# Performance work log

Hardware: AMD Instinct MI355X
Metric: run time of the kernel (lower is better)

The kernel has to match this reference:

```python
import jax, jax.numpy as jnp
import numpy as np


def setup_inputs() -> dict:
    key = jax.random.key(0)
    ks = jax.random.split(key, 9)
    B, C, H, W = 4, 256, 128, 128
    d = C // 8
    x = jax.random.normal(ks[0], (B, C, H, W), jnp.float32)
    wq = jax.random.normal(ks[1], (d, C), jnp.float32) * 0.05
    bq = jax.random.normal(ks[2], (d,), jnp.float32) * 0.05
    wk = jax.random.normal(ks[3], (d, C), jnp.float32) * 0.05
    bk = jax.random.normal(ks[4], (d,), jnp.float32) * 0.05
    wv = jax.random.normal(ks[5], (d, C), jnp.float32) * 0.05
    bv = jax.random.normal(ks[6], (d,), jnp.float32) * 0.05
    wp = jax.random.normal(ks[7], (C, d, 3, 3), jnp.float32) * 0.05
    gamma = jax.random.normal(ks[8], (1,), jnp.float32)
    return dict(x=x, wq=wq, bq=bq, wk=wk, bk=bk, wv=wv, bv=bv, wp=wp, gamma=gamma)


def reference(x, wq, bq, wk, bk, wv, bv, wp, gamma):
    B, C, H, W = x.shape
    d = wq.shape[0]  # C // 8
    N = H * W
    # 1x1 convs expressed as channel matmuls
    q = jnp.einsum('bchw,dc->bdhw', x, wq) + bq[None, :, None, None]
    k = jnp.einsum('bchw,dc->bdhw', x, wk) + bk[None, :, None, None]
    v = jnp.einsum('bchw,dc->bdhw', x, wv) + bv[None, :, None, None]
    Q = q.reshape(B, d, N)
    K = k.reshape(B, d, N)
    V = v.reshape(B, d, N)
    # channel-channel energy: [B, d, d]
    energy = jnp.einsum('bdn,ben->bde', Q, K)
    energy_new = jnp.max(energy, axis=-1, keepdims=True) - energy
    attention = jax.nn.softmax(energy_new, axis=-1)
    out = jnp.einsum('bde,ben->bdn', attention, V).reshape(B, d, H, W)
    # 3x3 conv (no bias) + exact GELU
    out = jax.lax.conv_general_dilated(
        out, wp, window_strides=(1, 1), padding='SAME',
        dimension_numbers=('NCHW', 'OIHW', 'NCHW'))
    out = jax.nn.gelu(out, approximate=False)
    return gamma[0] * out + x
```

## Files before the change

### kernel.cpp

```cpp
#include <hip/hip_runtime.h>
#include <hip/hip_bf16.h>
#include <math.h>

#define BB 4
#define CC 256
#define HH 128
#define WW 128
#define NN (HH*WW)
#define DD 32

#define AOT_CI   44
#define AOT_ROWE (130*AOT_CI)
#define AOT_IMGE (130*AOT_ROWE)
#define AOT_BYTES ((size_t)BB*AOT_IMGE*2)
#define AOT_ALLOC (AOT_BYTES + 1024)

#define WT_BYTES (9*256*AOT_CI*2)

#define PATCH_SZ 45760
#define WSLAB    22528
#define CONV_LDS (PATCH_SZ + 2*WSLAB)
#define EPI_PITCH 260

#define ASWZ_BYTES 98304
#define QKVP 260
#define QKV_LDS 131584

typedef __attribute__((ext_vector_type(8)))  short bf16x8;
typedef __attribute__((ext_vector_type(4)))  float f32x4;
typedef __attribute__((ext_vector_type(16))) float f32x16;

__device__ inline void async_copy16(void* lds, const void* g) {
    __builtin_amdgcn_global_load_lds(
        (const __attribute__((address_space(1))) unsigned int*)g,
        (__attribute__((address_space(3))) unsigned int*)lds, 16, 0, 0);
}

__device__ inline unsigned short f2bf(float f) {
    __hip_bfloat16 h = __float2bfloat16(f);
    return *reinterpret_cast<unsigned short*>(&h);
}

__device__ inline void split2(float v, unsigned short& h, unsigned short& l) {
    __hip_bfloat16 hb = __float2bfloat16(v);
    float r = v - __bfloat162float(hb);
    __hip_bfloat16 lb = __float2bfloat16(r);
    h = *reinterpret_cast<unsigned short*>(&hb);
    l = *reinterpret_cast<unsigned short*>(&lb);
}

__device__ inline unsigned int packsplit(float v) {
    unsigned int fb = __float_as_uint(v);
    unsigned int hb = fb & 0xFFFF0000u;
    float r = v - __uint_as_float(hb);
    unsigned int lb = __float_as_uint(r) >> 16;
    return (hb >> 16) | (lb << 16);
}

__device__ inline bf16x8 ld_frag8(const char* p) {
    union { bf16x8 v; short4 h[2]; } u;
    u.h[0] = *(const short4*)(p);
    u.h[1] = *(const short4*)(p + 8);
    return u.v;
}

__device__ inline float gelu_fast(float v) {
    float a = fabsf(v) * 0.70710678118654752f;
    float t = __fdividef(1.0f, fmaf(0.3275911f, a, 1.0f));
    float p = t * fmaf(t, fmaf(t, fmaf(t, fmaf(t, 1.061405429f, -1.453152027f),
                                       1.421413741f), -0.284496736f), 0.254829592f);
    float e = 1.0f - p * __expf(-a * a);
    float erfv = (v < 0.0f) ? -e : e;
    return 0.5f * v * (1.0f + erfv);
}

__global__ __launch_bounds__(256) void prep_kernel(
    const float* __restrict__ wp, unsigned short* __restrict__ Wt,
    const float* __restrict__ wq, const float* __restrict__ wk,
    const float* __restrict__ wv, unsigned short* __restrict__ Aswz,
    unsigned short* __restrict__ AOT)
{
    const int blk = blockIdx.x;
    if (blk < 288) {
        int i = blk*256 + threadIdx.x;
        int kk = i / (256*32);
        int r  = i % (256*32);
        int co = r >> 5, ci = r & 31;
        float v = wp[((size_t)co*32 + ci)*9 + kk];
        Wt[((size_t)kk*256 + co)*AOT_CI + ci] = f2bf(v);
    } else if (blk < 480) {
        int i = (blk-288)*256 + threadIdx.x;
        int j    = i & 7;
        int lane = (i >> 3) & 63;
        int q9   = i >> 9;
        int cf   = q9 % 3;
        int t    = q9 / 3;
        int hl   = t & 1;
        int s    = t >> 1;
        int row  = cf*32 + (lane & 31);
        int c    = s*16 + (lane >> 5)*8 + j;
        float w  = (row < 32) ? wq[row*256 + c]
                 : (row < 64) ? wk[(row-32)*256 + c]
                              : wv[(row-64)*256 + c];
        unsigned short h, l;
        split2(w, h, l);
        Aswz[i] = hl ? l : h;
    } else {
        int idx = (blk-480)*256 + threadIdx.x;
        if (idx < BB*22704) {
            int b = idx / 22704;
            int r = idx % 22704;
            size_t off;
            if (r < 11440) {
                int row = (r < 5720) ? 0 : 129;
                int e   = (r < 5720) ? r : r - 5720;
                off = (size_t)b*AOT_IMGE + (size_t)row*AOT_ROWE + e;
            } else {
                int r2 = r - 11440;
                int rr = r2 / 88 + 1;
                int w2 = r2 % 88;
                int col = (w2 < 44) ? 0 : 129;
                int ci  = (w2 < 44) ? w2 : w2 - 44;
                off = (size_t)b*AOT_IMGE + (size_t)rr*AOT_ROWE
                    + (size_t)col*AOT_CI + ci;
            }
            AOT[off] = 0;
        }
    }
}

__global__ __launch_bounds__(512, 1) void qkv_mfma_kernel(
    const float* __restrict__ x, const unsigned short* __restrict__ Aswz,
    const float* __restrict__ bq, const float* __restrict__ bk,
    const float* __restrict__ bv,
    float* __restrict__ Vout, float* __restrict__ Ep)
{
    __shared__ __align__(16) char lds[QKV_LDS];
    const int b    = blockIdx.y;
    const int s    = blockIdx.x;
    const int n0   = s * 256;
    const int tid  = threadIdx.x;
    const int w    = tid >> 6;
    const int lane = tid & 63;
    const int l31  = lane & 31;
    const int lh   = lane >> 5;
    const int ch_a = tid >> 6;
    const int f4   = tid & 63;

    for (int i = tid; i < 6144; i += 512)
        async_copy16(lds + i*16, (const char*)Aswz + i*16);
    float* biasL = (float*)(lds + 131072);
    if (tid < 96)
        biasL[tid] = (tid < 32) ? bq[tid] : (tid < 64) ? bk[tid-32] : bv[tid-64];

    unsigned int* stg[2] = { (unsigned int*)(lds + 98304),
                             (unsigned int*)(lds + 114688) };
    const float* xb = x + (size_t)b*CC*NN + n0 + f4*4;

    f32x16 acc0 = {0}, acc1 = {0}, acc2 = {0};

    float4 va0, vb0, va1, vb1, va2, vb2;
    #define LOADX(VA, VB, R) do { \
        VA = *(const float4*)(xb + (size_t)((R)*16 + ch_a    )*NN); \
        VB = *(const float4*)(xb + (size_t)((R)*16 + ch_a + 8)*NN); } while (0)
    #define PACKW(BUF, VA, VB) do { \
        uint4 ua, ub; \
        ua.x = packsplit((VA).x); ua.y = packsplit((VA).y); \
        ua.z = packsplit((VA).z); ua.w = packsplit((VA).w); \
        ub.x = packsplit((VB).x); ub.y = packsplit((VB).y); \
        ub.z = packsplit((VB).z); ub.w = packsplit((VB).w); \
        *(uint4*)((BUF) + (ch_a    )*256 + f4*4) = ua; \
        *(uint4*)((BUF) + (ch_a + 8)*256 + f4*4) = ub; } while (0)

    LOADX(va0, vb0, 0);
    LOADX(va1, vb1, 1);
    LOADX(va2, vb2, 2);
    PACKW(stg[0], va0, vb0);
    __syncthreads();

    #pragma unroll
    for (int r = 0; r < 16; ++r) {
        {
            const unsigned int* bufc = stg[r & 1];
            unsigned int u[8];
            #pragma unroll
            for (int j = 0; j < 8; ++j)
                u[j] = bufc[(lh*8 + j)*256 + 32*w + l31];
            union { bf16x8 v; unsigned int d[4]; } B1, B2;
            #pragma unroll
            for (int dq = 0; dq < 4; ++dq) {
                B1.d[dq] = (u[2*dq] & 0xFFFFu)      | (u[2*dq+1] << 16);
                B2.d[dq] = (u[2*dq] >> 16)          | (u[2*dq+1] & 0xFFFF0000u);
            }
            #pragma unroll
            for (int cf = 0; cf < 3; ++cf) {
                bf16x8 ah = *(const bf16x8*)(lds + (((r*6 +     cf)*64) + lane)*16);
                bf16x8 al = *(const bf16x8*)(lds + (((r*6 + 3 + cf)*64) + lane)*16);
                f32x16* ac = (cf == 0) ? &acc0 : (cf == 1) ? &acc1 : &acc2;
                *ac = __builtin_amdgcn_mfma_f32_32x32x16_bf16(ah, B1.v, *ac, 0, 0, 0);
                *ac = __builtin_amdgcn_mfma_f32_32x32x16_bf16(ah, B2.v, *ac, 0, 0, 0);
                *ac = __builtin_amdgcn_mfma_f32_32x32x16_bf16(al, B1.v, *ac, 0, 0, 0);
                *ac = __builtin_amdgcn_mfma_f32_32x32x16_bf16(al, B2.v, *ac, 0, 0, 0);
            }
        }
        if (r < 15) {
            if ((r+1) % 3 == 0)      PACKW(stg[(r+1) & 1], va0, vb0);
            else if ((r+1) % 3 == 1) PACKW(stg[(r+1) & 1], va1, vb1);
            else                     PACKW(stg[(r+1) & 1], va2, vb2);
        }
        if (r + 3 < 16) {
            if ((r+3) % 3 == 0)      LOADX(va0, vb0, r+3);
            else if ((r+3) % 3 == 1) LOADX(va1, vb1, r+3);
            else                     LOADX(va2, vb2, r+3);
        }
        __syncthreads();
    }

    float* qk = (float*)lds;
    #pragma unroll
    for (int r = 0; r < 16; ++r) {
        const int rsub = (r & 3) + 8*(r >> 2) + 4*lh;
        const int col  = 32*w + l31;
        qk[rsub*QKVP + col]      = acc0[r] + biasL[rsub];
        qk[(32+rsub)*QKVP + col] = acc1[r] + biasL[32 + rsub];
        Vout[((size_t)b*DD + rsub)*NN + n0 + col] = acc2[r] + biasL[64 + rsub];
    }
    __syncthreads();

    const int d  = tid >> 4;
    const int e2 = tid & 15;
    const float* qrow = qk + d*QKVP;
    float s0 = 0.f, s1 = 0.f;
    for (int n4 = 0; n4 < 256; n4 += 4) {
        float4 qv = *(const float4*)(qrow + n4);
        float4 ka = *(const float4*)(qk + (32 + e2)*QKVP + n4);
        float4 kb = *(const float4*)(qk + (48 + e2)*QKVP + n4);
        s0 += qv.x*ka.x + qv.y*ka.y + qv.z*ka.z + qv.w*ka.w;
        s1 += qv.x*kb.x + qv.y*kb.y + qv.z*kb.z + qv.w*kb.w;
    }
    float* ep = Ep + ((size_t)s*BB + b)*1024;
    ep[d*32 + e2]      = s0;
    ep[d*32 + e2 + 16] = s1;
    #undef LOADX
    #undef PACKW
}

__global__ __launch_bounds__(1024) void softmax_kernel(
    const float* __restrict__ Ep, float* __restrict__ attT)
{
    const int b = blockIdx.x;
    const int e = threadIdx.x, d = threadIdx.y;
    float s = 0.f;
    #pragma unroll 8
    for (int p = 0; p < 64; ++p)
        s += Ep[((size_t)p * BB + b) * (DD * DD) + d * DD + e];
    float nv = -s;
    float m = nv;
    for (int off = 16; off > 0; off >>= 1) m = fmaxf(m, __shfl_xor(m, off, 32));
    float pe = expf(nv - m);
    float su = pe;
    for (int off = 16; off > 0; off >>= 1) su += __shfl_xor(su, off, 32);
    attT[(size_t)b * (DD * DD) + e * DD + d] = pe / su;
}

__global__ __launch_bounds__(256) void pv_kernel(
    const float* __restrict__ V, const float* __restrict__ attT,
    unsigned short* __restrict__ AOT)
{
    __shared__ float Vs[DD][128];
    __shared__ float at4[DD][DD];
    const int b  = blockIdx.y;
    const int n0 = blockIdx.x * 128;
    const int tid = threadIdx.x;
    for (int i = tid; i < 1024; i += 256) {
        int r = i >> 5, c4 = i & 31;
        *(float4*)&Vs[r][c4*4] =
            *(const float4*)(V + ((size_t)b*DD + r)*NN + n0 + c4*4);
    }
    for (int i = tid; i < 1024; i += 256)
        at4[i >> 5][i & 31] = attT[(size_t)b*1024 + i];
    __syncthreads();
    const int nl = tid & 127;
    const int dg = tid >> 7;
    float acc[16];
    #pragma unroll
    for (int k = 0; k < 16; ++k) acc[k] = 0.f;
    #pragma unroll 4
    for (int e = 0; e < DD; ++e) {
        float v = Vs[e][nl];
        const float4* ar = (const float4*)&at4[e][dg*16];
        #pragma unroll
        for (int q = 0; q < 4; ++q) {
            float4 a = ar[q];
            acc[4*q+0] += a.x * v; acc[4*q+1] += a.y * v;
            acc[4*q+2] += a.z * v; acc[4*q+3] += a.w * v;
        }
    }
    const int n = n0 + nl;
    const int h = n >> 7, ww = n & 127;
    unsigned short* dst = AOT + (size_t)b*AOT_IMGE + (size_t)(h+1)*AOT_ROWE
                              + (size_t)(ww+1)*AOT_CI + dg*16;
    #pragma unroll
    for (int q = 0; q < 4; ++q) {
        ushort4 u;
        u.x = f2bf(acc[4*q+0]); u.y = f2bf(acc[4*q+1]);
        u.z = f2bf(acc[4*q+2]); u.w = f2bf(acc[4*q+3]);
        *(ushort4*)(dst + 4*q) = u;
    }
}

__global__ __launch_bounds__(512, 1) void conv_kernel(
    const unsigned short* __restrict__ AOT, const unsigned short* __restrict__ Wt,
    const float* __restrict__ gammap, const float* __restrict__ x,
    float* __restrict__ out)
{
    __shared__ __align__(16) char lds[CONV_LDS];
    const int b   = blockIdx.y;
    const int h0  = blockIdx.x * 2;
    const int tid = threadIdx.x;
    const int wid = tid >> 6;
    const int lane = tid & 63;
    const int l15 = lane & 15;
    const int lj  = lane >> 4;
    const int wn  = wid & 1;
    const int wc  = wid >> 1;

    const char* psrc = (const char*)(AOT + (size_t)b*AOT_IMGE + (size_t)h0*AOT_ROWE);
    for (int i = tid; i < PATCH_SZ/16; i += 512)
        async_copy16(lds + i*16, psrc + i*16);
    for (int i = tid; i < WSLAB/16; i += 512)
        async_copy16(lds + PATCH_SZ + i*16, (const char*)Wt + i*16);
    __syncthreads();

    f32x4 acc[4][8];
    #pragma unroll
    for (int cf = 0; cf < 4; ++cf)
        #pragma unroll
        for (int nf = 0; nf < 8; ++nf)
            acc[cf][nf] = (f32x4){0.f, 0.f, 0.f, 0.f};

    for (int kk = 0; kk < 9; ++kk) {
        if (kk < 8) {
            const char* wsrc = (const char*)Wt + (size_t)(kk+1)*WSLAB;
            char* wdst = lds + PATCH_SZ + ((kk+1)&1)*WSLAB;
            for (int i = tid; i < WSLAB/16; i += 512)
                async_copy16(wdst + i*16, wsrc + i*16);
        }
        const int kh = kk / 3, kw = kk % 3;
        const char* wbase = lds + PATCH_SZ + (kk&1)*WSLAB;
        bf16x8 af[4];
        #pragma unroll
        for (int cf = 0; cf < 4; ++cf)
            af[cf] = ld_frag8(wbase + (wc*64 + cf*16 + l15)*88 + lj*16);
        #pragma unroll
        for (int nf = 0; nf < 8; ++nf) {
            const int cell = (wn + kh)*130 + nf*16 + l15 + kw;
            const bf16x8 bfr = ld_frag8(lds + cell*88 + lj*16);
            #pragma unroll
            for (int cf = 0; cf < 4; ++cf)
                acc[cf][nf] = __builtin_amdgcn_mfma_f32_16x16x32_bf16(
                    af[cf], bfr, acc[cf][nf], 0, 0, 0);
        }
        __syncthreads();
    }

    const float g0 = gammap[0];
    float* lf = (float*)lds;
    for (int k = 0; k < 4; ++k) {
        if (wc == k) {
            #pragma unroll
            for (int cf = 0; cf < 4; ++cf) {
                const int rl = cf*16 + 4*lj;
                #pragma unroll
                for (int nf = 0; nf < 8; ++nf) {
                    const int col = wn*128 + nf*16 + l15;
                    #pragma unroll
                    for (int j = 0; j < 4; ++j)
                        lf[(rl + j)*EPI_PITCH + col] = acc[cf][nf][j];
                }
            }
        }
        __syncthreads();
        #pragma unroll
        for (int it = 0; it < 8; ++it) {
            const int idx = tid + it*512;
            const int row = idx >> 6, c4 = idx & 63;
            const int co  = k*64 + row;
            const size_t g = ((size_t)b*CC + co)*NN + (size_t)h0*WW + c4*4;
            float4 v  = *(const float4*)(lf + row*EPI_PITCH + c4*4);
            float4 xv = *(const float4*)(x + g);
            float4 o;
            o.x = g0*gelu_fast(v.x) + xv.x;
            o.y = g0*gelu_fast(v.y) + xv.y;
            o.z = g0*gelu_fast(v.z) + xv.z;
            o.w = g0*gelu_fast(v.w) + xv.w;
            *(float4*)(out + g) = o;
        }
        __syncthreads();
    }
}

extern "C" void kernel_launch(void* const* d_in, const int* in_sizes, int n_in,
                              void* d_out, int out_size, void* d_ws, size_t ws_size,
                              hipStream_t stream)
{
    const float* x  = (const float*)d_in[0];
    const float* wq = (const float*)d_in[1];
    const float* bq = (const float*)d_in[2];
    const float* wk = (const float*)d_in[3];
    const float* bk = (const float*)d_in[4];
    const float* wv = (const float*)d_in[5];
    const float* bv = (const float*)d_in[6];
    const float* wp = (const float*)d_in[7];
    const float* gm = (const float*)d_in[8];
    float* out = (float*)d_out;

    float* Vbuf = out;

    char* ws = (char*)d_ws;
    unsigned short* AOT  = (unsigned short*)ws;
    unsigned short* Wt   = (unsigned short*)(ws + AOT_ALLOC);
    unsigned short* Aswz = (unsigned short*)(ws + AOT_ALLOC + WT_BYTES);
    float* Ep  = (float*)(ws + AOT_ALLOC + WT_BYTES + ASWZ_BYTES);
    float* ATT = Ep + (size_t)64*BB*1024;

    prep_kernel    <<<dim3(1024), 256, 0, stream>>>(wp, Wt, wq, wk, wv, Aswz, AOT);
    qkv_mfma_kernel<<<dim3(64, BB), 512, 0, stream>>>(x, Aswz, bq, bk, bv, Vbuf, Ep);
    softmax_kernel <<<dim3(BB), dim3(32, 32), 0, stream>>>(Ep, ATT);
    pv_kernel      <<<dim3(128, BB), 256, 0, stream>>>(Vbuf, ATT, AOT);
    conv_kernel    <<<dim3(64, BB), 512, 0, stream>>>(AOT, Wt, gm, x, out);
}
```

Baseline: 79.89 us.

## Fuse QKV, softmax and PV into one cooperative kernel with grid sync

Merges the QKV projection, channel softmax and attention-times-V kernels into one cooperative kernel that uses a grid-wide barrier after writing partial energies. V stays in registers instead of making a round trip through global memory, and two kernel launches go away. Each block recomputes the softmax for its batch redundantly from the partial sums, then applies the attention matrix to its register-resident V tile and writes bf16 into the padded conv input. The prep grid size also changes. The change depends on all 256 blocks being co-resident for the grid sync, and launch bounds are raised to 2 blocks per CU even though the kernel uses about 131KB of LDS per block.

Result: slower. 161.8 us (+102.5%).

```diff
diff --git a/kernel.cpp b/kernel.cpp
--- a/kernel.cpp
+++ b/kernel.cpp
@@ -1,5 +1,6 @@
 #include <hip/hip_runtime.h>
 #include <hip/hip_bf16.h>
+#include <hip/hip_cooperative_groups.h>
 #include <math.h>
 
 #define BB 4
@@ -29,6 +30,8 @@
 typedef __attribute__((ext_vector_type(8)))  short bf16x8;
 typedef __attribute__((ext_vector_type(4)))  float f32x4;
 typedef __attribute__((ext_vector_type(16))) float f32x16;
+
+namespace cg = cooperative_groups;
 
 __device__ inline void async_copy16(void* lds, const void* g) {
     __builtin_amdgcn_global_load_lds(
@@ -129,11 +132,11 @@
     }
 }
 
-__global__ __launch_bounds__(512, 1) void qkv_mfma_kernel(
+__global__ __launch_bounds__(512, 2) void fused_attn_kernel(
     const float* __restrict__ x, const unsigned short* __restrict__ Aswz,
     const float* __restrict__ bq, const float* __restrict__ bk,
     const float* __restrict__ bv,
-    float* __restrict__ Vout, float* __restrict__ Ep)
+    float* __restrict__ Ep, unsigned short* __restrict__ AOT)
 {
     __shared__ __align__(16) char lds[QKV_LDS];
     const int b    = blockIdx.y;
@@ -189,8 +192,8 @@
             union { bf16x8 v; unsigned int d[4]; } B1, B2;
             #pragma unroll
             for (int dq = 0; dq < 4; ++dq) {
-                B1.d[dq] = (u[2*dq] & 0xFFFFu)      | (u[2*dq+1] << 16);
-                B2.d[dq] = (u[2*dq] >> 16)          | (u[2*dq+1] & 0xFFFF0000u);
+                B1.d[dq] = (u[2*dq] & 0xFFFFu) | (u[2*dq+1] << 16);
+                B2.d[dq] = (u[2*dq] >> 16)     | (u[2*dq+1] & 0xFFFF0000u);
             }
             #pragma unroll
             for (int cf = 0; cf < 3; ++cf) {
@@ -215,6 +218,8 @@
         }
         __syncthreads();
     }
+    #undef LOADX
+    #undef PACKW
 
     float* qk = (float*)lds;
     #pragma unroll
@@ -223,89 +228,85 @@
         const int col  = 32*w + l31;
         qk[rsub*QKVP + col]      = acc0[r] + biasL[rsub];
         qk[(32+rsub)*QKVP + col] = acc1[r] + biasL[32 + rsub];
-        Vout[((size_t)b*DD + rsub)*NN + n0 + col] = acc2[r] + biasL[64 + rsub];
     }
     __syncthreads();
 
-    const int d  = tid >> 4;
-    const int e2 = tid & 15;
-    const float* qrow = qk + d*QKVP;
-    float s0 = 0.f, s1 = 0.f;
-    for (int n4 = 0; n4 < 256; n4 += 4) {
-        float4 qv = *(const float4*)(qrow + n4);
-        float4 ka = *(const float4*)(qk + (32 + e2)*QKVP + n4);
-        float4 kb = *(const float4*)(qk + (48 + e2)*QKVP + n4);
-        s0 += qv.x*ka.x + qv.y*ka.y + qv.z*ka.z + qv.w*ka.w;
-        s1 += qv.x*kb.x + qv.y*kb.y + qv.z*kb.z + qv.w*kb.w;
-    }
-    float* ep = Ep + ((size_t)s*BB + b)*1024;
-    ep[d*32 + e2]      = s0;
-    ep[d*32 + e2 + 16] = s1;
-    #undef LOADX
-    #undef PACKW
-}
-
-__global__ __launch_bounds__(1024) void softmax_kernel(
-    const float* __restrict__ Ep, float* __restrict__ attT)
-{
-    const int b = blockIdx.x;
-    const int e = threadIdx.x, d = threadIdx.y;
-    float s = 0.f;
-    #pragma unroll 8
-    for (int p = 0; p < 64; ++p)
-        s += Ep[((size_t)p * BB + b) * (DD * DD) + d * DD + e];
-    float nv = -s;
-    float m = nv;
-    for (int off = 16; off > 0; off >>= 1) m = fmaxf(m, __shfl_xor(m, off, 32));
-    float pe = expf(nv - m);
-    float su = pe;
-    for (int off = 16; off > 0; off >>= 1) su += __shfl_xor(su, off, 32);
-    attT[(size_t)b * (DD * DD) + e * DD + d] = pe / su;
-}
-
-__global__ __launch_bounds__(256) void pv_kernel(
-    const float* __restrict__ V, const float* __restrict__ attT,
-    unsigned short* __restrict__ AOT)
-{
-    __shared__ float Vs[DD][128];
-    __shared__ float at4[DD][DD];
-    const int b  = blockIdx.y;
-    const int n0 = blockIdx.x * 128;
-    const int tid = threadIdx.x;
-    for (int i = tid; i < 1024; i += 256) {
-        int r = i >> 5, c4 = i & 31;
-        *(float4*)&Vs[r][c4*4] =
-            *(const float4*)(V + ((size_t)b*DD + r)*NN + n0 + c4*4);
-    }
-    for (int i = tid; i < 1024; i += 256)
-        at4[i >> 5][i & 31] = attT[(size_t)b*1024 + i];
+    {
+        const int d  = tid >> 4;
+        const int e2 = tid & 15;
+        const float* qrow = qk + d*QKVP;
+        float s0 = 0.f, s1 = 0.f;
+        for (int n4 = 0; n4 < 256; n4 += 4) {
+            float4 qv = *(const float4*)(qrow + n4);
+            float4 ka = *(const float4*)(qk + (32 + e2)*QKVP + n4);
+            float4 kb = *(const float4*)(qk + (48 + e2)*QKVP + n4);
+            s0 += qv.x*ka.x + qv.y*ka.y + qv.z*ka.z + qv.w*ka.w;
+            s1 += qv.x*kb.x + qv.y*kb.y + qv.z*kb.z + qv.w*kb.w;
+        }
+        float* ep = Ep + ((size_t)s*BB + b)*1024;
+        ep[d*32 + e2]      = s0;
+        ep[d*32 + e2 + 16] = s1;
+    }
+
+    __threadfence();
+    cg::this_grid().sync();
+
+    float* at4 = (float*)(lds + 98304);
+    {
+        float e0s = 0.f, e1s = 0.f;
+        #pragma unroll 8
+        for (int p = 0; p < 64; ++p) {
+            float2 v = *(const float2*)(Ep + ((size_t)p*BB + b)*1024 + 2*tid);
+            e0s += v.x; e1s += v.y;
+        }
+        float nv0 = -e0s, nv1 = -e1s;
+        float m = fmaxf(nv0, nv1);
+        for (int off = 8; off > 0; off >>= 1) m = fmaxf(m, __shfl_xor(m, off, 16));
+        float p0 = expf(nv0 - m), p1 = expf(nv1 - m);
+        float su = p0 + p1;
+        for (int off = 8; off > 0; off >>= 1) su += __shfl_xor(su, off, 16);
+        const float inv = 1.0f / su;
+        const int d = tid >> 4;
+        const int e = 2*(tid & 15);
+        at4[e*36 + d]     = p0 * inv;
+        at4[(e+1)*36 + d] = p1 * inv;
+    }
     __syncthreads();
-    const int nl = tid & 127;
-    const int dg = tid >> 7;
-    float acc[16];
-    #pragma unroll
-    for (int k = 0; k < 16; ++k) acc[k] = 0.f;
-    #pragma unroll 4
-    for (int e = 0; e < DD; ++e) {
-        float v = Vs[e][nl];
-        const float4* ar = (const float4*)&at4[e][dg*16];
+
+    {
+        float accd[32];
+        #pragma unroll
+        for (int d = 0; d < 32; ++d) accd[d] = 0.f;
+        #pragma unroll
+        for (int r = 0; r < 16; ++r) {
+            const int rsub = (r & 3) + 8*(r >> 2) + 4*lh;
+            const float v = acc2[r] + biasL[64 + rsub];
+            const float4* ar = (const float4*)(at4 + rsub*36);
+            #pragma unroll
+            for (int dq = 0; dq < 8; ++dq) {
+                float4 a = ar[dq];
+                accd[4*dq+0] += a.x * v; accd[4*dq+1] += a.y * v;
+                accd[4*dq+2] += a.z * v; accd[4*dq+3] += a.w * v;
+            }
+        }
+        #pragma unroll
+        for (int d = 0; d < 32; ++d)
+            accd[d] += __shfl_xor(accd[d], 32);
+        float fin[16];
+        #pragma unroll
+        for (int j = 0; j < 16; ++j)
+            fin[j] = lh ? accd[16 + j] : accd[j];
+        const int n  = n0 + 32*w + l31;
+        const int h  = n >> 7, ww = n & 127;
+        unsigned short* dst = AOT + (size_t)b*AOT_IMGE + (size_t)(h+1)*AOT_ROWE
+                                  + (size_t)(ww+1)*AOT_CI + 16*lh;
         #pragma unroll
         for (int q = 0; q < 4; ++q) {
-            float4 a = ar[q];
-            acc[4*q+0] += a.x * v; acc[4*q+1] += a.y * v;
-            acc[4*q+2] += a.z * v; acc[4*q+3] += a.w * v;
-        }
-    }
-    const int n = n0 + nl;
-    const int h = n >> 7, ww = n & 127;
-    unsigned short* dst = AOT + (size_t)b*AOT_IMGE + (size_t)(h+1)*AOT_ROWE
-                              + (size_t)(ww+1)*AOT_CI + dg*16;
-    #pragma unroll
-    for (int q = 0; q < 4; ++q) {
-        ushort4 u;
-        u.x = f2bf(acc[4*q+0]); u.y = f2bf(acc[4*q+1]);
-        u.z = f2bf(acc[4*q+2]); u.w = f2bf(acc[4*q+3]);
-        *(ushort4*)(dst + 4*q) = u;
+            ushort4 u;
+            u.x = f2bf(fin[4*q+0]); u.y = f2bf(fin[4*q+1]);
+            u.z = f2bf(fin[4*q+2]); u.w = f2bf(fin[4*q+3]);
+            *(ushort4*)(dst + 4*q) = u;
+        }
     }
 }
 
@@ -415,18 +416,20 @@
     const float* gm = (const float*)d_in[8];
     float* out = (float*)d_out;
 
-    float* Vbuf = out;
-
     char* ws = (char*)d_ws;
     unsigned short* AOT  = (unsigned short*)ws;
     unsigned short* Wt   = (unsigned short*)(ws + AOT_ALLOC);
     unsigned short* Aswz = (unsigned short*)(ws + AOT_ALLOC + WT_BYTES);
-    float* Ep  = (float*)(ws + AOT_ALLOC + WT_BYTES + ASWZ_BYTES);
-    float* ATT = Ep + (size_t)64*BB*1024;
-
-    prep_kernel    <<<dim3(1024), 256, 0, stream>>>(wp, Wt, wq, wk, wv, Aswz, AOT);
-    qkv_mfma_kernel<<<dim3(64, BB), 512, 0, stream>>>(x, Aswz, bq, bk, bv, Vbuf, Ep);
-    softmax_kernel <<<dim3(BB), dim3(32, 32), 0, stream>>>(Ep, ATT);
-    pv_kernel      <<<dim3(128, BB), 256, 0, stream>>>(Vbuf, ATT, AOT);
-    conv_kernel    <<<dim3(64, BB), 512, 0, stream>>>(AOT, Wt, gm, x, out);
-}
+    float* Ep = (float*)(ws + AOT_ALLOC + WT_BYTES + ASWZ_BYTES);
+
+    prep_kernel<<<dim3(835), 256, 0, stream>>>(wp, Wt, wq, wk, wv, Aswz, AOT);
+
+    {
+        void* args[] = { (void*)&x, (void*)&Aswz, (void*)&bq, (void*)&bk,
+                         (void*)&bv, (void*)&Ep, (void*)&AOT };
+        hipLaunchCooperativeKernel((void*)fused_attn_kernel,
+                                   dim3(64, BB), dim3(512), args, 0, stream);
+    }
+
+    conv_kernel<<<dim3(64, BB), 512, 0, stream>>>(AOT, Wt, gm, x, out);
+}
```

## Use per-wave staging buffers in QKV kernel to drop per-iteration barriers

Applied to the files above, without the earlier changes.

The QKV MFMA kernel now gives each wave a private double-buffered LDS slab holding only the 32 spatial columns it consumes. The per-iteration __syncthreads in the 16-step channel loop can therefore be removed, and the next global load of x is issued before the MFMA work. The intent is to cut block-wide barrier stalls and improve overlap of loads with compute. It relies on in-wave ordering of LDS writes and reads. The prep kernel grid also shrinks from 1024 to 835 blocks, which is only safe if its work partition matches.

New measurement: 79.88 us. Within noise of the previous version (-0.0%).

```diff
diff --git a/kernel.cpp b/kernel.cpp
--- a/kernel.cpp
+++ b/kernel.cpp
@@ -144,8 +144,8 @@
     const int lane = tid & 63;
     const int l31  = lane & 31;
     const int lh   = lane >> 5;
-    const int ch_a = tid >> 6;
-    const int f4   = tid & 63;
+    const int chl  = lane >> 3;
+    const int nq   = lane & 7;
 
     for (int i = tid; i < 6144; i += 512)
         async_copy16(lds + i*16, (const char*)Aswz + i*16);
@@ -153,44 +153,49 @@
     if (tid < 96)
         biasL[tid] = (tid < 32) ? bq[tid] : (tid < 64) ? bk[tid-32] : bv[tid-64];
 
-    unsigned int* stg[2] = { (unsigned int*)(lds + 98304),
-                             (unsigned int*)(lds + 114688) };
-    const float* xb = x + (size_t)b*CC*NN + n0 + f4*4;
+    char* mybuf = lds + 98304 + w*4096;
+    const float* xq4 = x + (size_t)b*CC*NN + n0 + 32*w + nq*4;
 
     f32x16 acc0 = {0}, acc1 = {0}, acc2 = {0};
 
-    float4 va0, vb0, va1, vb1, va2, vb2;
+    float4 sa0, sb0, sa1, sb1, sa2, sb2;
     #define LOADX(VA, VB, R) do { \
-        VA = *(const float4*)(xb + (size_t)((R)*16 + ch_a    )*NN); \
-        VB = *(const float4*)(xb + (size_t)((R)*16 + ch_a + 8)*NN); } while (0)
-    #define PACKW(BUF, VA, VB) do { \
+        VA = *(const float4*)(xq4 + (size_t)((R)*16 + chl    )*NN); \
+        VB = *(const float4*)(xq4 + (size_t)((R)*16 + 8 + chl)*NN); } while (0)
+    #define PACKW(R, VA, VB) do { \
+        unsigned int* bp = (unsigned int*)(mybuf + ((R) & 1)*2048); \
         uint4 ua, ub; \
         ua.x = packsplit((VA).x); ua.y = packsplit((VA).y); \
         ua.z = packsplit((VA).z); ua.w = packsplit((VA).w); \
         ub.x = packsplit((VB).x); ub.y = packsplit((VB).y); \
         ub.z = packsplit((VB).z); ub.w = packsplit((VB).w); \
-        *(uint4*)((BUF) + (ch_a    )*256 + f4*4) = ua; \
-        *(uint4*)((BUF) + (ch_a + 8)*256 + f4*4) = ub; } while (0)
-
-    LOADX(va0, vb0, 0);
-    LOADX(va1, vb1, 1);
-    LOADX(va2, vb2, 2);
-    PACKW(stg[0], va0, vb0);
+        *(uint4*)(bp + (chl    )*32 + nq*4) = ua; \
+        *(uint4*)(bp + (8 + chl)*32 + nq*4) = ub; } while (0)
+
+    LOADX(sa0, sb0, 0);
+    LOADX(sa1, sb1, 1);
+    LOADX(sa2, sb2, 2);
+    PACKW(0, sa0, sb0);
     __syncthreads();
 
     #pragma unroll
     for (int r = 0; r < 16; ++r) {
+        if (r + 3 < 16) {
+            if ((r+3) % 3 == 0)      LOADX(sa0, sb0, r+3);
+            else if ((r+3) % 3 == 1) LOADX(sa1, sb1, r+3);
+            else                     LOADX(sa2, sb2, r+3);
+        }
         {
-            const unsigned int* bufc = stg[r & 1];
+            const unsigned int* bufc = (const unsigned int*)(mybuf + (r & 1)*2048);
             unsigned int u[8];
             #pragma unroll
             for (int j = 0; j < 8; ++j)
-                u[j] = bufc[(lh*8 + j)*256 + 32*w + l31];
+                u[j] = bufc[(lh*8 + j)*32 + l31];
             union { bf16x8 v; unsigned int d[4]; } B1, B2;
             #pragma unroll
             for (int dq = 0; dq < 4; ++dq) {
-                B1.d[dq] = (u[2*dq] & 0xFFFFu)      | (u[2*dq+1] << 16);
-                B2.d[dq] = (u[2*dq] >> 16)          | (u[2*dq+1] & 0xFFFF0000u);
+                B1.d[dq] = (u[2*dq] & 0xFFFFu) | (u[2*dq+1] << 16);
+                B2.d[dq] = (u[2*dq] >> 16)     | (u[2*dq+1] & 0xFFFF0000u);
             }
             #pragma unroll
             for (int cf = 0; cf < 3; ++cf) {
@@ -203,19 +208,16 @@
                 *ac = __builtin_amdgcn_mfma_f32_32x32x16_bf16(al, B2.v, *ac, 0, 0, 0);
             }
         }
-        if (r < 15) {
-            if ((r+1) % 3 == 0)      PACKW(stg[(r+1) & 1], va0, vb0);
-            else if ((r+1) % 3 == 1) PACKW(stg[(r+1) & 1], va1, vb1);
-            else                     PACKW(stg[(r+1) & 1], va2, vb2);
-        }
-        if (r + 3 < 16) {
-            if ((r+3) % 3 == 0)      LOADX(va0, vb0, r+3);
-            else if ((r+3) % 3 == 1) LOADX(va1, vb1, r+3);
-            else                     LOADX(va2, vb2, r+3);
-        }
-        __syncthreads();
-    }
-
+        if (r + 1 < 16) {
+            if ((r+1) % 3 == 0)      PACKW(r+1, sa0, sb0);
+            else if ((r+1) % 3 == 1) PACKW(r+1, sa1, sb1);
+            else                     PACKW(r+1, sa2, sb2);
+        }
+    }
+    #undef LOADX
+    #undef PACKW
+
+    __syncthreads();
     float* qk = (float*)lds;
     #pragma unroll
     for (int r = 0; r < 16; ++r) {
@@ -241,8 +243,6 @@
     float* ep = Ep + ((size_t)s*BB + b)*1024;
     ep[d*32 + e2]      = s0;
     ep[d*32 + e2 + 16] = s1;
-    #undef LOADX
-    #undef PACKW
 }
 
 __global__ __launch_bounds__(1024) void softmax_kernel(
@@ -424,7 +424,7 @@
     float* Ep  = (float*)(ws + AOT_ALLOC + WT_BYTES + ASWZ_BYTES);
     float* ATT = Ep + (size_t)64*BB*1024;
 
-    prep_kernel    <<<dim3(1024), 256, 0, stream>>>(wp, Wt, wq, wk, wv, Aswz, AOT);
+    prep_kernel    <<<dim3(835), 256, 0, stream>>>(wp, Wt, wq, wk, wv, Aswz, AOT);
     qkv_mfma_kernel<<<dim3(64, BB), 512, 0, stream>>>(x, Aswz, bq, bk, bv, Vbuf, Ep);
     softmax_kernel <<<dim3(BB), dim3(32, 32), 0, stream>>>(Ep, ATT);
     pv_kernel      <<<dim3(128, BB), 256, 0, stream>>>(Vbuf, ATT, AOT);
```
